# Optimization experiments

Measured on AMD Instinct MI355X. Metric: run time of the kernel, lower is better.

Reference implementation:

```python
import jax, jax.numpy as jnp
import numpy as np

N_TOKENS = 16384
IN_FEATURES = 1024
OUT_FEATURES = 1024
BH = 32  # block rows (out dim)
BW = 32  # block cols (in dim)
N_BLOCKS = 256  # density 0.25 * (1024*1024/(32*32))


def setup_inputs() -> dict:
    key = jax.random.key(0)
    k1, k2, k3, k4 = jax.random.split(key, 4)
    x = jax.random.normal(k1, (N_TOKENS, IN_FEATURES), dtype=jnp.float32)
    weight_data = jax.random.normal(k2, (N_BLOCKS, BH, BW), dtype=jnp.float32)
    bias = jnp.zeros((OUT_FEATURES,), dtype=jnp.float32)
    block_row = jax.random.randint(k3, (N_BLOCKS,), 0, OUT_FEATURES // BH, dtype=jnp.int32)
    block_col = jax.random.randint(k4, (N_BLOCKS,), 0, IN_FEATURES // BW, dtype=jnp.int32)
    return {"x": x, "weight_data": weight_data, "bias": bias,
            "block_row": block_row, "block_col": block_col}


def reference(x, weight_data, bias, block_row, block_col):
    # Block-sparse linear: y = x @ W^T + bias, with W[out, in] stored as
    # N_BLOCKS dense (BH, BW) blocks at (block_row, block_col) block coords.
    N = x.shape[0]
    B, bh, bw = weight_data.shape
    n_row_blocks = bias.shape[0] // bh
    x3 = x.reshape(N, -1, bw)           # [N, in/bw, bw]
    xb = x3[:, block_col, :]            # gather input block-columns: [N, B, bw]
    # per-block partial output rows: data[b] @ x_colblock -> [N, B, bh]
    partial = jnp.einsum('nbw,bow->nbo', xb, weight_data)
    y3 = jnp.zeros((N, n_row_blocks, bh), dtype=x.dtype).at[:, block_row, :].add(partial)
    return y3.reshape(N, -1) + bias
```

## Files before the change

kernel.cpp:

```cpp
#include <hip/hip_runtime.h>

#define N_TOKENS 16384
#define IN_F 1024
#define OUT_F 1024
#define NB 256
#define BH 32
#define BW 32
#define NRB 32
#define T_TILE 32
#define NW 8
#define XS_STRIDE 1040
#define SCHED_ALLOC 304
#define WF_SLOT_SHORTS 1024
#define FLUSH_BIT (1 << 10)

#define WS_WF_BYTES   (SCHED_ALLOC * WF_SLOT_SHORTS * 2)
#define WS_SCHED_OFF  WS_WF_BYTES
#define WS_POS_OFF    (WS_SCHED_OFF + SCHED_ALLOC * 4)
#define WS_WSTART_OFF (WS_POS_OFF + NB * 4)

typedef short short8 __attribute__((ext_vector_type(8)));
typedef float float4v __attribute__((ext_vector_type(4)));

__device__ __forceinline__ short f2bf(float f) {
    unsigned u = __builtin_bit_cast(unsigned, f);
    u += 0x7fffu + ((u >> 16) & 1u);
    return (short)(u >> 16);
}

__global__ void prep_sched_kernel(const int* __restrict__ brow, const int* __restrict__ bcol,
                                  int* __restrict__ sched, int* __restrict__ pos_of,
                                  int* __restrict__ wstart, short* __restrict__ wf)
{
    __shared__ int cnt[NRB], start[NRB], cur[NRB];
    __shared__ int eff[NRB], rnk[NRB], wv[NRB], off[NRB];
    __shared__ int wtot[NW], pw[NW + 1];
    const int tid = threadIdx.x;
    if (tid < NRB) { cnt[tid] = 0; cur[tid] = 0; }
    __syncthreads();
    const int r = brow[tid];
    const int c = bcol[tid];
    atomicAdd(&cnt[r], 1);
    __syncthreads();
    if (tid < NRB) eff[tid] = cnt[tid] ? cnt[tid] : 1;
    __syncthreads();
    if (tid < NRB) {
        const int e_ = eff[tid];
        int rk = 0;
        for (int j = 0; j < NRB; ++j) {
            const int ej = eff[j];
            if (ej > e_ || (ej == e_ && j < tid)) ++rk;
        }
        rnk[tid] = rk;
        const int s8 = rk & 7, dir = (rk >> 3) & 1;
        wv[tid] = dir ? (7 - s8) : s8;
    }
    __syncthreads();
    if (tid < NRB) {
        const int w = wv[tid], rk = rnk[tid];
        int o = 0;
        for (int j = 0; j < NRB; ++j)
            if (wv[j] == w && rnk[j] < rk) o += eff[j];
        off[tid] = o;
    }
    if (tid >= NRB && tid < NRB + NW) {
        const int w = tid - NRB;
        int t = 0;
        for (int j = 0; j < NRB; ++j) if (wv[j] == w) t += eff[j];
        wtot[w] = t;
    }
    __syncthreads();
    if (tid == 0) {
        int ws = 0;
        for (int w = 0; w < NW; ++w) { pw[w] = ws; ws += (wtot[w] + 1) & ~1; }
        pw[NW] = ws;
        for (int q = 0; q < 8; ++q) sched[ws + q] = 0;
    }
    __syncthreads();
    if (tid < NRB) start[tid] = pw[wv[tid]] + off[tid];
    if (tid < NW) {
        wstart[tid] = pw[tid];
        if (wtot[tid] & 1) sched[pw[tid] + wtot[tid]] = 0;
    }
    if (tid == NW) wstart[NW] = pw[NW];
    __syncthreads();
    const int slot = atomicAdd(&cur[r], 1);
    const int pos = start[r] + slot;
    sched[pos] = c | (r << 5) | ((slot == cnt[r] - 1) ? FLUSH_BIT : 0);
    pos_of[tid] = pos;
    if (tid < NRB && cnt[tid] == 0) {
        sched[start[tid]] = (tid << 5) | FLUSH_BIT;
        int4 z = {0, 0, 0, 0};
        int4* dst = (int4*)(wf + (size_t)start[tid] * WF_SLOT_SHORTS);
        for (int q = 0; q < WF_SLOT_SHORTS / 8; ++q) dst[q] = z;
    }
}

__global__ void prep_w_kernel(const float* __restrict__ wd, const int* __restrict__ pos_of,
                              short* __restrict__ wf)
{
    const int g = blockIdx.x * blockDim.x + threadIdx.x;
    const int lane = g & 63;
    const int oh = (g >> 6) & 1;
    const int b = g >> 7;
    const int l16 = lane & 15, quad = lane >> 4;
    const int pos = pos_of[b];
    const float* src = wd + (size_t)b * (BH * BW) + (oh * 16 + l16) * BW + quad * 8;
    const float4 w0 = *(const float4*)src;
    const float4 w1 = *(const float4*)(src + 4);
    short8 o;
    o[0] = f2bf(w0.x); o[1] = f2bf(w0.y); o[2] = f2bf(w0.z); o[3] = f2bf(w0.w);
    o[4] = f2bf(w1.x); o[5] = f2bf(w1.y); o[6] = f2bf(w1.z); o[7] = f2bf(w1.w);
    *(short8*)(wf + (size_t)pos * WF_SLOT_SHORTS + oh * 512 + lane * 8) = o;
}

__global__ __launch_bounds__(512, 4) void spmm_main_kernel(
    const float* __restrict__ x, const float* __restrict__ bias,
    const short* __restrict__ wf, const int* __restrict__ sched_g,
    const int* __restrict__ wstart_g, float* __restrict__ out)
{
    __shared__ short xs[T_TILE * XS_STRIDE];
    __shared__ float sbias[OUT_F];
    __shared__ int ssched[SCHED_ALLOC];

    const int tid = threadIdx.x;
    const int n0 = blockIdx.x * T_TILE;
    const int lane = tid & 63;
    const int wave = tid >> 6;
    const int l16 = lane & 15, quad = lane >> 4;

    const int s = __builtin_amdgcn_readfirstlane(wstart_g[wave]);
    const int e = __builtin_amdgcn_readfirstlane(wstart_g[wave + 1]);
    int e0 = __builtin_amdgcn_readfirstlane(sched_g[s]);
    int e1 = __builtin_amdgcn_readfirstlane(sched_g[s + 1]);
    int e2 = __builtin_amdgcn_readfirstlane(sched_g[s + 2]);
    int e3 = __builtin_amdgcn_readfirstlane(sched_g[s + 3]);
    const short* wfl = wf + lane * 8;
    short8 cwA0 = *(const short8*)(wfl + (size_t)s * WF_SLOT_SHORTS);
    short8 cwB0 = *(const short8*)(wfl + (size_t)s * WF_SLOT_SHORTS + 512);
    short8 cwA1 = *(const short8*)(wfl + (size_t)(s + 1) * WF_SLOT_SHORTS);
    short8 cwB1 = *(const short8*)(wfl + (size_t)(s + 1) * WF_SLOT_SHORTS + 512);
    short8 nwA0 = *(const short8*)(wfl + (size_t)(s + 2) * WF_SLOT_SHORTS);
    short8 nwB0 = *(const short8*)(wfl + (size_t)(s + 2) * WF_SLOT_SHORTS + 512);
    short8 nwA1 = *(const short8*)(wfl + (size_t)(s + 3) * WF_SLOT_SHORTS);
    short8 nwB1 = *(const short8*)(wfl + (size_t)(s + 3) * WF_SLOT_SHORTS + 512);

    {
        const int tr = tid >> 7;
        const int tc = tid & 127;
        const float* xp = x + (size_t)(n0 + tr) * IN_F + tc * 8;
        short* sp = xs + tr * XS_STRIDE + tc * 8;
#pragma unroll
        for (int it = 0; it < T_TILE / 4; ++it) {
            const float4 a = *(const float4*)xp;
            const float4 b = *(const float4*)(xp + 4);
            short8 sv;
            sv[0] = f2bf(a.x); sv[1] = f2bf(a.y); sv[2] = f2bf(a.z); sv[3] = f2bf(a.w);
            sv[4] = f2bf(b.x); sv[5] = f2bf(b.y); sv[6] = f2bf(b.z); sv[7] = f2bf(b.w);
            *(short8*)sp = sv;
            xp += 4 * IN_F;
            sp += 4 * XS_STRIDE;
        }
    }
    if (tid < SCHED_ALLOC) ssched[tid] = sched_g[tid];
    if (tid < OUT_F / 4) *(float4*)(sbias + tid * 4) = *(const float4*)(bias + tid * 4);
    __syncthreads();

    const short* x0 = xs + l16 * XS_STRIDE + quad * 8;
    const short* x1 = x0 + 16 * XS_STRIDE;
    short8 a0t0 = *(const short8*)(x0 + (e0 & 31) * BW);
    short8 a0t1 = *(const short8*)(x1 + (e0 & 31) * BW);
    short8 a1t0 = *(const short8*)(x0 + (e1 & 31) * BW);
    short8 a1t1 = *(const short8*)(x1 + (e1 & 31) * BW);

    float4v accA = {0.f, 0.f, 0.f, 0.f};
    float4v accB = {0.f, 0.f, 0.f, 0.f};
    float4v accC = {0.f, 0.f, 0.f, 0.f};
    float4v accD = {0.f, 0.f, 0.f, 0.f};
    float* const outb = out + (size_t)(n0 + quad * 4) * OUT_F + l16;

    auto flush = [&](int ev) {
        if (ev & FLUSH_BIT) {
            const int rr = (ev >> 5) & 31;
            const int ob = rr * BH;
            const float bv0 = sbias[ob + l16];
            const float bv1 = sbias[ob + 16 + l16];
            float* op0 = outb + ob;
            float* op1 = op0 + (size_t)16 * OUT_F;
#pragma unroll
            for (int g = 0; g < 4; ++g) {
                __builtin_nontemporal_store(accA[g] + bv0, &op0[(size_t)g * OUT_F]);
                __builtin_nontemporal_store(accB[g] + bv1, &op0[(size_t)g * OUT_F + 16]);
                __builtin_nontemporal_store(accC[g] + bv0, &op1[(size_t)g * OUT_F]);
                __builtin_nontemporal_store(accD[g] + bv1, &op1[(size_t)g * OUT_F + 16]);
            }
            accA = (float4v){0.f, 0.f, 0.f, 0.f};
            accB = (float4v){0.f, 0.f, 0.f, 0.f};
            accC = (float4v){0.f, 0.f, 0.f, 0.f};
            accD = (float4v){0.f, 0.f, 0.f, 0.f};
        }
    };

    for (int k = s; k < e; k += 2) {
        const int e4 = __builtin_amdgcn_readfirstlane(ssched[k + 4]);
        const int e5 = __builtin_amdgcn_readfirstlane(ssched[k + 5]);
        const short8 fwA0 = *(const short8*)(wfl + (size_t)(k + 4) * WF_SLOT_SHORTS);
        const short8 fwB0 = *(const short8*)(wfl + (size_t)(k + 4) * WF_SLOT_SHORTS + 512);
        const short8 fwA1 = *(const short8*)(wfl + (size_t)(k + 5) * WF_SLOT_SHORTS);
        const short8 fwB1 = *(const short8*)(wfl + (size_t)(k + 5) * WF_SLOT_SHORTS + 512);
        const short8 na0t0 = *(const short8*)(x0 + (e2 & 31) * BW);
        const short8 na0t1 = *(const short8*)(x1 + (e2 & 31) * BW);
        const short8 na1t0 = *(const short8*)(x0 + (e3 & 31) * BW);
        const short8 na1t1 = *(const short8*)(x1 + (e3 & 31) * BW);

        accA = __builtin_amdgcn_mfma_f32_16x16x32_bf16(a0t0, cwA0, accA, 0, 0, 0);
        accB = __builtin_amdgcn_mfma_f32_16x16x32_bf16(a0t0, cwB0, accB, 0, 0, 0);
        accC = __builtin_amdgcn_mfma_f32_16x16x32_bf16(a0t1, cwA0, accC, 0, 0, 0);
        accD = __builtin_amdgcn_mfma_f32_16x16x32_bf16(a0t1, cwB0, accD, 0, 0, 0);
        flush(e0);
        accA = __builtin_amdgcn_mfma_f32_16x16x32_bf16(a1t0, cwA1, accA, 0, 0, 0);
        accB = __builtin_amdgcn_mfma_f32_16x16x32_bf16(a1t0, cwB1, accB, 0, 0, 0);
        accC = __builtin_amdgcn_mfma_f32_16x16x32_bf16(a1t1, cwA1, accC, 0, 0, 0);
        accD = __builtin_amdgcn_mfma_f32_16x16x32_bf16(a1t1, cwB1, accD, 0, 0, 0);
        flush(e1);

        e0 = e2; e1 = e3; e2 = e4; e3 = e5;
        a0t0 = na0t0; a0t1 = na0t1; a1t0 = na1t0; a1t1 = na1t1;
        cwA0 = nwA0; cwB0 = nwB0; cwA1 = nwA1; cwB1 = nwB1;
        nwA0 = fwA0; nwB0 = fwB0; nwA1 = fwA1; nwB1 = fwB1;
    }
}

extern "C" void kernel_launch(void* const* d_in, const int* in_sizes, int n_in,
                              void* d_out, int out_size, void* d_ws, size_t ws_size,
                              hipStream_t stream) {
    const float* x    = (const float*)d_in[0];
    const float* wd   = (const float*)d_in[1];
    const float* bias = (const float*)d_in[2];
    const int* brow   = (const int*)d_in[3];
    const int* bcol   = (const int*)d_in[4];
    float* out = (float*)d_out;

    char* ws = (char*)d_ws;
    short* wf   = (short*)ws;
    int* sched  = (int*)(ws + WS_SCHED_OFF);
    int* pos_of = (int*)(ws + WS_POS_OFF);
    int* wstart = (int*)(ws + WS_WSTART_OFF);

    prep_sched_kernel<<<1, 256, 0, stream>>>(brow, bcol, sched, pos_of, wstart, wf);
    prep_w_kernel<<<NB * 128 / 256, 256, 0, stream>>>(wd, pos_of, wf);
    spmm_main_kernel<<<N_TOKENS / T_TILE, 512, 0, stream>>>(x, bias, wf, sched, wstart, out);
}
```

Measured before the change: 138.6 us.

## Interleave per-wave schedule and stream weights into LDS via global_load_lds double buffer

The schedule is rebuilt so that each wave's blocks are interleaved (entry t*NW+wave) and every wave is padded to a common length L with zero weight slots. The main kernel now double-buffers the weight fragments in LDS using direct global-to-LDS loads, prefetching the next step while computing the current one, with a block-wide barrier every step. It also drops the bias LDS staging and reads bias from global at flush, and lowers the occupancy hint from 4 to 2. The goal is to hide weight-fetch latency with fewer VGPRs. The cost is a __syncthreads per block step, padding work that makes every wave run as long as the longest one, and no wait on the async LDS load before the barrier.

```diff
diff --git a/kernel.cpp b/kernel.cpp
--- a/kernel.cpp
+++ b/kernel.cpp
@@ -10,7 +10,7 @@
 #define T_TILE 32
 #define NW 8
 #define XS_STRIDE 1040
-#define SCHED_ALLOC 304
+#define SCHED_ALLOC 344
 #define WF_SLOT_SHORTS 1024
 #define FLUSH_BIT (1 << 10)
 
@@ -28,13 +28,20 @@
     return (short)(u >> 16);
 }
 
+__device__ __forceinline__ void gld16(const short* g, short* l) {
+    __builtin_amdgcn_global_load_lds(
+        (const __attribute__((address_space(1))) unsigned int*)g,
+        (__attribute__((address_space(3))) unsigned int*)l, 16, 0, 0);
+}
+
 __global__ void prep_sched_kernel(const int* __restrict__ brow, const int* __restrict__ bcol,
                                   int* __restrict__ sched, int* __restrict__ pos_of,
                                   int* __restrict__ wstart, short* __restrict__ wf)
 {
-    __shared__ int cnt[NRB], start[NRB], cur[NRB];
+    __shared__ int cnt[NRB], cur[NRB];
     __shared__ int eff[NRB], rnk[NRB], wv[NRB], off[NRB];
-    __shared__ int wtot[NW], pw[NW + 1];
+    __shared__ int wlen[NW];
+    __shared__ int Lsh;
     const int tid = threadIdx.x;
     if (tid < NRB) { cnt[tid] = 0; cur[tid] = 0; }
     __syncthreads();
@@ -51,8 +58,8 @@
             const int ej = eff[j];
             if (ej > e_ || (ej == e_ && j < tid)) ++rk;
         }
+        const int s8 = rk & 7, dir = (rk >> 3) & 1;
         rnk[tid] = rk;
-        const int s8 = rk & 7, dir = (rk >> 3) & 1;
         wv[tid] = dir ? (7 - s8) : s8;
     }
     __syncthreads();
@@ -67,32 +74,37 @@
         const int w = tid - NRB;
         int t = 0;
         for (int j = 0; j < NRB; ++j) if (wv[j] == w) t += eff[j];
-        wtot[w] = t;
+        wlen[w] = t;
     }
     __syncthreads();
     if (tid == 0) {
-        int ws = 0;
-        for (int w = 0; w < NW; ++w) { pw[w] = ws; ws += (wtot[w] + 1) & ~1; }
-        pw[NW] = ws;
-        for (int q = 0; q < 8; ++q) sched[ws + q] = 0;
-    }
-    __syncthreads();
-    if (tid < NRB) start[tid] = pw[wv[tid]] + off[tid];
-    if (tid < NW) {
-        wstart[tid] = pw[tid];
-        if (wtot[tid] & 1) sched[pw[tid] + wtot[tid]] = 0;
-    }
-    if (tid == NW) wstart[NW] = pw[NW];
-    __syncthreads();
+        int L = 0;
+        for (int w = 0; w < NW; ++w) L = wlen[w] > L ? wlen[w] : L;
+        if (L * NW > SCHED_ALLOC) L = SCHED_ALLOC / NW;
+        Lsh = L;
+        wstart[0] = L;
+    }
+    __syncthreads();
+    const int L = Lsh;
     const int slot = atomicAdd(&cur[r], 1);
-    const int pos = start[r] + slot;
+    const int pos = (off[r] + slot) * NW + wv[r];
     sched[pos] = c | (r << 5) | ((slot == cnt[r] - 1) ? FLUSH_BIT : 0);
     pos_of[tid] = pos;
     if (tid < NRB && cnt[tid] == 0) {
-        sched[start[tid]] = (tid << 5) | FLUSH_BIT;
+        const int p2 = off[tid] * NW + wv[tid];
+        sched[p2] = (tid << 5) | FLUSH_BIT;
         int4 z = {0, 0, 0, 0};
-        int4* dst = (int4*)(wf + (size_t)start[tid] * WF_SLOT_SHORTS);
+        int4* dst = (int4*)(wf + (size_t)p2 * WF_SLOT_SHORTS);
         for (int q = 0; q < WF_SLOT_SHORTS / 8; ++q) dst[q] = z;
+    }
+    for (int p = tid; p < NW * L; p += 256) {
+        const int w = p & 7, j = p >> 3;
+        if (j >= wlen[w]) {
+            sched[p] = 0;
+            int4 z = {0, 0, 0, 0};
+            int4* dst = (int4*)(wf + (size_t)p * WF_SLOT_SHORTS);
+            for (int q = 0; q < WF_SLOT_SHORTS / 8; ++q) dst[q] = z;
+        }
     }
 }
 
@@ -114,13 +126,13 @@
     *(short8*)(wf + (size_t)pos * WF_SLOT_SHORTS + oh * 512 + lane * 8) = o;
 }
 
-__global__ __launch_bounds__(512, 4) void spmm_main_kernel(
+__global__ __launch_bounds__(512, 2) void spmm_main_kernel(
     const float* __restrict__ x, const float* __restrict__ bias,
     const short* __restrict__ wf, const int* __restrict__ sched_g,
     const int* __restrict__ wstart_g, float* __restrict__ out)
 {
     __shared__ short xs[T_TILE * XS_STRIDE];
-    __shared__ float sbias[OUT_F];
+    __shared__ short wfb[2][NW][1024];
     __shared__ int ssched[SCHED_ALLOC];
 
     const int tid = threadIdx.x;
@@ -129,21 +141,13 @@
     const int wave = tid >> 6;
     const int l16 = lane & 15, quad = lane >> 4;
 
-    const int s = __builtin_amdgcn_readfirstlane(wstart_g[wave]);
-    const int e = __builtin_amdgcn_readfirstlane(wstart_g[wave + 1]);
-    int e0 = __builtin_amdgcn_readfirstlane(sched_g[s]);
-    int e1 = __builtin_amdgcn_readfirstlane(sched_g[s + 1]);
-    int e2 = __builtin_amdgcn_readfirstlane(sched_g[s + 2]);
-    int e3 = __builtin_amdgcn_readfirstlane(sched_g[s + 3]);
-    const short* wfl = wf + lane * 8;
-    short8 cwA0 = *(const short8*)(wfl + (size_t)s * WF_SLOT_SHORTS);
-    short8 cwB0 = *(const short8*)(wfl + (size_t)s * WF_SLOT_SHORTS + 512);
-    short8 cwA1 = *(const short8*)(wfl + (size_t)(s + 1) * WF_SLOT_SHORTS);
-    short8 cwB1 = *(const short8*)(wfl + (size_t)(s + 1) * WF_SLOT_SHORTS + 512);
-    short8 nwA0 = *(const short8*)(wfl + (size_t)(s + 2) * WF_SLOT_SHORTS);
-    short8 nwB0 = *(const short8*)(wfl + (size_t)(s + 2) * WF_SLOT_SHORTS + 512);
-    short8 nwA1 = *(const short8*)(wfl + (size_t)(s + 3) * WF_SLOT_SHORTS);
-    short8 nwB1 = *(const short8*)(wfl + (size_t)(s + 3) * WF_SLOT_SHORTS + 512);
+    const int L = __builtin_amdgcn_readfirstlane(wstart_g[0]);
+
+    {
+        const short* g0 = wf + (size_t)(0 * NW + wave) * WF_SLOT_SHORTS + lane * 8;
+        gld16(g0,       &wfb[0][wave][0]);
+        gld16(g0 + 512, &wfb[0][wave][512]);
+    }
 
     {
         const int tr = tid >> 7;
@@ -163,15 +167,10 @@
         }
     }
     if (tid < SCHED_ALLOC) ssched[tid] = sched_g[tid];
-    if (tid < OUT_F / 4) *(float4*)(sbias + tid * 4) = *(const float4*)(bias + tid * 4);
     __syncthreads();
 
     const short* x0 = xs + l16 * XS_STRIDE + quad * 8;
     const short* x1 = x0 + 16 * XS_STRIDE;
-    short8 a0t0 = *(const short8*)(x0 + (e0 & 31) * BW);
-    short8 a0t1 = *(const short8*)(x1 + (e0 & 31) * BW);
-    short8 a1t0 = *(const short8*)(x0 + (e1 & 31) * BW);
-    short8 a1t1 = *(const short8*)(x1 + (e1 & 31) * BW);
 
     float4v accA = {0.f, 0.f, 0.f, 0.f};
     float4v accB = {0.f, 0.f, 0.f, 0.f};
@@ -183,8 +182,8 @@
         if (ev & FLUSH_BIT) {
             const int rr = (ev >> 5) & 31;
             const int ob = rr * BH;
-            const float bv0 = sbias[ob + l16];
-            const float bv1 = sbias[ob + 16 + l16];
+            const float bv0 = bias[ob + l16];
+            const float bv1 = bias[ob + 16 + l16];
             float* op0 = outb + ob;
             float* op1 = op0 + (size_t)16 * OUT_F;
 #pragma unroll
@@ -201,33 +200,25 @@
         }
     };
 
-    for (int k = s; k < e; k += 2) {
-        const int e4 = __builtin_amdgcn_readfirstlane(ssched[k + 4]);
-        const int e5 = __builtin_amdgcn_readfirstlane(ssched[k + 5]);
-        const short8 fwA0 = *(const short8*)(wfl + (size_t)(k + 4) * WF_SLOT_SHORTS);
-        const short8 fwB0 = *(const short8*)(wfl + (size_t)(k + 4) * WF_SLOT_SHORTS + 512);
-        const short8 fwA1 = *(const short8*)(wfl + (size_t)(k + 5) * WF_SLOT_SHORTS);
-        const short8 fwB1 = *(const short8*)(wfl + (size_t)(k + 5) * WF_SLOT_SHORTS + 512);
-        const short8 na0t0 = *(const short8*)(x0 + (e2 & 31) * BW);
-        const short8 na0t1 = *(const short8*)(x1 + (e2 & 31) * BW);
-        const short8 na1t0 = *(const short8*)(x0 + (e3 & 31) * BW);
-        const short8 na1t1 = *(const short8*)(x1 + (e3 & 31) * BW);
-
-        accA = __builtin_amdgcn_mfma_f32_16x16x32_bf16(a0t0, cwA0, accA, 0, 0, 0);
-        accB = __builtin_amdgcn_mfma_f32_16x16x32_bf16(a0t0, cwB0, accB, 0, 0, 0);
-        accC = __builtin_amdgcn_mfma_f32_16x16x32_bf16(a0t1, cwA0, accC, 0, 0, 0);
-        accD = __builtin_amdgcn_mfma_f32_16x16x32_bf16(a0t1, cwB0, accD, 0, 0, 0);
-        flush(e0);
-        accA = __builtin_amdgcn_mfma_f32_16x16x32_bf16(a1t0, cwA1, accA, 0, 0, 0);
-        accB = __builtin_amdgcn_mfma_f32_16x16x32_bf16(a1t0, cwB1, accB, 0, 0, 0);
-        accC = __builtin_amdgcn_mfma_f32_16x16x32_bf16(a1t1, cwA1, accC, 0, 0, 0);
-        accD = __builtin_amdgcn_mfma_f32_16x16x32_bf16(a1t1, cwB1, accD, 0, 0, 0);
-        flush(e1);
-
-        e0 = e2; e1 = e3; e2 = e4; e3 = e5;
-        a0t0 = na0t0; a0t1 = na0t1; a1t0 = na1t0; a1t1 = na1t1;
-        cwA0 = nwA0; cwB0 = nwB0; cwA1 = nwA1; cwB1 = nwB1;
-        nwA0 = fwA0; nwB0 = fwB0; nwA1 = fwA1; nwB1 = fwB1;
+    int buf = 0;
+    for (int t = 0; t < L; ++t) {
+        if (t + 1 < L) {
+            const short* g = wf + (size_t)((t + 1) * NW + wave) * WF_SLOT_SHORTS + lane * 8;
+            gld16(g,       &wfb[buf ^ 1][wave][0]);
+            gld16(g + 512, &wfb[buf ^ 1][wave][512]);
+        }
+        const int ev = __builtin_amdgcn_readfirstlane(ssched[t * NW + wave]);
+        const short8 wA = *(const short8*)&wfb[buf][wave][lane * 8];
+        const short8 wB = *(const short8*)&wfb[buf][wave][512 + lane * 8];
+        const short8 at0 = *(const short8*)(x0 + (ev & 31) * BW);
+        const short8 at1 = *(const short8*)(x1 + (ev & 31) * BW);
+        accA = __builtin_amdgcn_mfma_f32_16x16x32_bf16(at0, wA, accA, 0, 0, 0);
+        accB = __builtin_amdgcn_mfma_f32_16x16x32_bf16(at0, wB, accB, 0, 0, 0);
+        accC = __builtin_amdgcn_mfma_f32_16x16x32_bf16(at1, wA, accC, 0, 0, 0);
+        accD = __builtin_amdgcn_mfma_f32_16x16x32_bf16(at1, wB, accD, 0, 0, 0);
+        flush(ev);
+        __syncthreads();
+        buf ^= 1;
     }
 }
 
```

After: 160.7 us. +16.0%, slower.
